# Kernel tuning notes

Measured on AMD Instinct MI355X. Metric: run time of the kernel, lower is better.

Reference implementation:

```python
import jax, jax.numpy as jnp
import numpy as np
import math

N_HEADS = 8
EMBED = 128
HEAD_DEPTH = EMBED // N_HEADS
CLIP = 10.0
NEG_INF = 1.0e10
SCALE = math.sqrt(HEAD_DEPTH)


def setup_inputs() -> dict:
    key = jax.random.key(0)
    ks = jax.random.split(key, 8)
    B, C, N = 32, 2, 512
    Q = jax.random.normal(ks[0], (B, C, N, EMBED), dtype=jnp.float32)
    K = jax.random.normal(ks[1], (B, C, N, EMBED), dtype=jnp.float32)
    V = jax.random.normal(ks[2], (B, C, N, EMBED), dtype=jnp.float32)
    mask = jax.random.bernoulli(ks[3], 0.15, (B, C, N, 1))  # True = masked out
    stdv_qkv = 1.0 / math.sqrt(HEAD_DEPTH)
    stdv_out = 1.0 / math.sqrt(EMBED)
    # torch nn.Linear weights: (out_features, in_features)
    Wq = jax.random.uniform(ks[4], (EMBED, EMBED), jnp.float32, -stdv_qkv, stdv_qkv)
    Wk = jax.random.uniform(ks[5], (EMBED, EMBED), jnp.float32, -stdv_qkv, stdv_qkv)
    Wv = jax.random.uniform(ks[6], (EMBED, EMBED), jnp.float32, -stdv_qkv, stdv_qkv)
    Wout = jax.random.uniform(ks[7], (EMBED, EMBED), jnp.float32, -stdv_out, stdv_out)
    return {"Q": Q, "K": K, "V": V, "mask": mask,
            "Wq": Wq, "Wk": Wk, "Wv": Wv, "Wout": Wout}


def _split_heads(T):
    # (b, c, n, E) -> (b, H, c, n, d)
    b, c, n, _ = T.shape
    return T.reshape(b, c, n, N_HEADS, HEAD_DEPTH).transpose(0, 3, 1, 2, 4)


def reference(Q, K, V, mask, Wq, Wk, Wv, Wout):
    # Linear projections (torch Linear: y = x @ W.T)
    q = _split_heads(jnp.einsum('bcne,fe->bcnf', Q, Wq))
    k = _split_heads(jnp.einsum('bcne,fe->bcnf', K, Wk))
    v = _split_heads(jnp.einsum('bcne,fe->bcnf', V, Wv))
    # logits: (b, H, c, q, k)
    logits = jnp.einsum('bhcqd,bhckd->bhcqk', q, k) / SCALE
    logits = CLIP * jnp.tanh(logits)
    # mask (b, c, n, 1) -> (b, 1, c, 1, n); True -> -1e10
    m = mask[:, None, :, :, :].swapaxes(-1, -2)
    logits = jnp.where(m, -NEG_INF, logits)
    probs = jax.nn.softmax(logits, axis=-1)
    out = jnp.einsum('bhcqk,bhckd->bhcqd', probs, v)
    # combine heads: (b, H, c, n, d) -> (b, c, n, E)
    b, h, c, n, d = out.shape
    out = out.transpose(0, 2, 3, 1, 4).reshape(b, c, n, EMBED)
    return jnp.einsum('bcne,fe->bcnf', out, Wout)
```

## Files before the change

kernel.cpp:

```cpp
#include <hip/hip_runtime.h>

typedef _Float16 half_t;
typedef _Float16 half8 __attribute__((ext_vector_type(8)));
typedef _Float16 half4 __attribute__((ext_vector_type(4)));
typedef float floatx4 __attribute__((ext_vector_type(4)));
typedef float floatx16 __attribute__((ext_vector_type(16)));

#define C1 0.72134752044448170368f
#define C2 14.4269504088896340736f
#define C3 28.8539008177792681472f

__device__ __forceinline__ floatx4 zero4() {
    floatx4 z; z[0] = z[1] = z[2] = z[3] = 0.f; return z;
}
__device__ __forceinline__ floatx16 zero16() {
    floatx16 z;
#pragma unroll
    for (int i = 0; i < 16; ++i) z[i] = 0.f;
    return z;
}

__device__ __forceinline__ float pfun(float sp, float b) {
    float u = __builtin_amdgcn_exp2f(sp);
    float r = __builtin_amdgcn_rcpf(u + 1.0f);
    return __builtin_amdgcn_exp2f(b - C3 * r);
}

__global__ void k_convw(const float* __restrict__ Wq, const float* __restrict__ Wk,
                        const float* __restrict__ Wv, const float* __restrict__ Wo,
                        half_t* __restrict__ Wh) {
    int idx = blockIdx.x * 256 + threadIdx.x;
    int which = idx >> 14;
    int off = idx & 16383;
    const float* src = (which == 0) ? Wq : (which == 1) ? Wk : (which == 2) ? Wv : Wo;
    float scale = (which == 0) ? C1 : 1.0f;
    Wh[idx] = (half_t)(src[off] * scale);
}

__global__ __launch_bounds__(256) void k_proj(
        const float* __restrict__ Q, const float* __restrict__ K,
        const float* __restrict__ V, const half_t* __restrict__ WhBase,
        half_t* __restrict__ qw, half_t* __restrict__ kw, half_t* __restrict__ vw) {
    int which = blockIdx.y;
    const float* X = (which == 0) ? Q : (which == 1) ? K : V;
    const half_t* W = WhBase + which * 16384;

    int tid = threadIdx.x;
    int w = tid >> 6, lane = tid & 63;
    int l15 = lane & 15, quad = lane >> 4;
    int tokbase = blockIdx.x * 64 + w * 16;

    floatx4 acc[8];
#pragma unroll
    for (int nt = 0; nt < 8; ++nt) acc[nt] = zero4();

#pragma unroll
    for (int ks = 0; ks < 4; ++ks) {
        const float* ap = X + (tokbase + l15) * 128 + ks * 32 + quad * 8;
        float4 a0 = *(const float4*)ap;
        float4 a1 = *(const float4*)(ap + 4);
        half8 xf;
        xf[0] = (half_t)a0.x; xf[1] = (half_t)a0.y; xf[2] = (half_t)a0.z; xf[3] = (half_t)a0.w;
        xf[4] = (half_t)a1.x; xf[5] = (half_t)a1.y; xf[6] = (half_t)a1.z; xf[7] = (half_t)a1.w;
        if (which == 2) {
#pragma unroll
            for (int nt = 0; nt < 8; ++nt) {
                half8 wf = *(const half8*)(W + (nt * 16 + l15) * 128 + ks * 32 + quad * 8);
                acc[nt] = __builtin_amdgcn_mfma_f32_16x16x32_f16(xf, wf, acc[nt], 0, 0, 0);
            }
        } else {
#pragma unroll
            for (int nt = 0; nt < 8; ++nt) {
                half8 wf = *(const half8*)(W + (nt * 16 + l15) * 128 + ks * 32 + quad * 8);
                acc[nt] = __builtin_amdgcn_mfma_f32_16x16x32_f16(wf, xf, acc[nt], 0, 0, 0);
            }
        }
    }

    if (which == 2) {
        int R0 = tokbase + quad * 4;
        int bc = R0 >> 9, n0 = R0 & 511;
#pragma unroll
        for (int nt = 0; nt < 8; ++nt) {
            half4 hv;
            hv[0] = (half_t)acc[nt][0]; hv[1] = (half_t)acc[nt][1];
            hv[2] = (half_t)acc[nt][2]; hv[3] = (half_t)acc[nt][3];
            *(half4*)(vw + ((bc * 8 + nt) * 16 + l15) * 512 + n0) = hv;
        }
    } else {
        int R = tokbase + l15;
        int bc = R >> 9, n = R & 511;
        half_t* Y = (which == 0) ? qw : kw;
#pragma unroll
        for (int nt = 0; nt < 8; ++nt) {
            half4 hv;
            hv[0] = (half_t)acc[nt][0]; hv[1] = (half_t)acc[nt][1];
            hv[2] = (half_t)acc[nt][2]; hv[3] = (half_t)acc[nt][3];
            *(half4*)(Y + ((bc * 8 + nt) * 512 + n) * 16 + quad * 4) = hv;
        }
    }
}

__global__ __launch_bounds__(64, 8) void k_attn(
        const half_t* __restrict__ qg, const half_t* __restrict__ kg,
        const half_t* __restrict__ vTg, const int* __restrict__ mask,
        half_t* __restrict__ attn) {
    __shared__ float bias[512];
    __shared__ half_t Pb[32 * 36];

    int bx = blockIdx.x;
    int bch = bx >> 4, qt = bx & 15;
    int bc = bch >> 3, h = bch & 7;
    int lane = threadIdx.x;
    int l31 = lane & 31, hf = lane >> 5;
    int l15 = lane & 15, quad = lane >> 4;

    const half_t* qh = qg + bch * 8192;
    const half_t* kh = kg + bch * 8192;
    const half_t* vh = vTg + bch * 8192;

#pragma unroll
    for (int i = 0; i < 8; ++i)
        bias[i * 64 + lane] = mask[bc * 512 + i * 64 + lane] ? -1.0e30f : C2;
    __syncthreads();

    int qbase = qt * 32;
    half8 qf = *(const half8*)(qh + (qbase + l31) * 16 + hf * 8);

    half8 ones;
#pragma unroll
    for (int j = 0; j < 8; ++j) ones[j] = (half_t)1.0f;

    floatx4 O[2], Os[2];
    O[0] = zero4(); O[1] = zero4();
    Os[0] = zero4(); Os[1] = zero4();
    const float4* b4 = (const float4*)bias;

#pragma unroll 1
    for (int c = 0; c < 16; ++c) {
        half8 kf = *(const half8*)(kh + (c * 32 + l31) * 16 + hf * 8);
        half8 vf = *(const half8*)(vh + l15 * 512 + c * 32 + quad * 8);
        float4 bv[4];
#pragma unroll
        for (int g = 0; g < 4; ++g) bv[g] = b4[c * 8 + hf + 2 * g];

        floatx16 S = __builtin_amdgcn_mfma_f32_32x32x16_f16(kf, qf, zero16(), 0, 0, 0);
#pragma unroll
        for (int g = 0; g < 4; ++g) {
            float p0 = pfun(S[4 * g + 0], bv[g].x);
            float p1 = pfun(S[4 * g + 1], bv[g].y);
            float p2 = pfun(S[4 * g + 2], bv[g].z);
            float p3 = pfun(S[4 * g + 3], bv[g].w);
            auto t0 = __builtin_amdgcn_cvt_pkrtz(p0, p1);
            auto t1 = __builtin_amdgcn_cvt_pkrtz(p2, p3);
            half4 ph;
            ph[0] = (half_t)t0[0]; ph[1] = (half_t)t0[1];
            ph[2] = (half_t)t1[0]; ph[3] = (half_t)t1[1];
            *(half4*)(Pb + l31 * 36 + hf * 4 + g * 8) = ph;
        }
#pragma unroll
        for (int nt2 = 0; nt2 < 2; ++nt2) {
            half8 pb = *(const half8*)(Pb + (nt2 * 16 + l15) * 36 + quad * 8);
            O[nt2]  = __builtin_amdgcn_mfma_f32_16x16x32_f16(vf,   pb, O[nt2],  0, 0, 0);
            Os[nt2] = __builtin_amdgcn_mfma_f32_16x16x32_f16(ones, pb, Os[nt2], 0, 0, 0);
        }
    }

#pragma unroll
    for (int nt = 0; nt < 2; ++nt) {
        float iv = __builtin_amdgcn_rcpf(Os[nt][0]);
        int qrow = qbase + nt * 16 + l15;
        half4 ov;
        ov[0] = (half_t)(O[nt][0] * iv);
        ov[1] = (half_t)(O[nt][1] * iv);
        ov[2] = (half_t)(O[nt][2] * iv);
        ov[3] = (half_t)(O[nt][3] * iv);
        *(half4*)(attn + (bc * 512 + qrow) * 128 + h * 16 + quad * 4) = ov;
    }
}

__global__ __launch_bounds__(256) void k_out(
        const half_t* __restrict__ A, const half_t* __restrict__ Wh,
        float* __restrict__ out) {
    int tid = threadIdx.x;
    int w = tid >> 6, lane = tid & 63;
    int l15 = lane & 15, quad = lane >> 4;
    int tokbase = blockIdx.x * 64 + w * 16;

    floatx4 acc[8];
#pragma unroll
    for (int nt = 0; nt < 8; ++nt) acc[nt] = zero4();
#pragma unroll
    for (int ks = 0; ks < 4; ++ks) {
        half8 xf = *(const half8*)(A + (tokbase + l15) * 128 + ks * 32 + quad * 8);
#pragma unroll
        for (int nt = 0; nt < 8; ++nt) {
            half8 wf = *(const half8*)(Wh + (nt * 16 + l15) * 128 + ks * 32 + quad * 8);
            acc[nt] = __builtin_amdgcn_mfma_f32_16x16x32_f16(wf, xf, acc[nt], 0, 0, 0);
        }
    }
#pragma unroll
    for (int nt = 0; nt < 8; ++nt) {
        float4 o;
        o.x = acc[nt][0]; o.y = acc[nt][1]; o.z = acc[nt][2]; o.w = acc[nt][3];
        *(float4*)(out + (tokbase + l15) * 128 + nt * 16 + quad * 4) = o;
    }
}

extern "C" void kernel_launch(void* const* d_in, const int* in_sizes, int n_in,
                              void* d_out, int out_size, void* d_ws, size_t ws_size,
                              hipStream_t stream) {
    const float* Q    = (const float*)d_in[0];
    const float* K    = (const float*)d_in[1];
    const float* V    = (const float*)d_in[2];
    const int*   mask = (const int*)d_in[3];
    const float* Wq   = (const float*)d_in[4];
    const float* Wk   = (const float*)d_in[5];
    const float* Wv   = (const float*)d_in[6];
    const float* Wo   = (const float*)d_in[7];
    float* out = (float*)d_out;

    half_t* ws = (half_t*)d_ws;
    half_t* Wh = ws;
    half_t* qw = ws + 65536;
    half_t* kw = qw + 4194304;
    half_t* vw = kw + 4194304;
    half_t* aw = vw + 4194304;

    k_convw<<<256, 256, 0, stream>>>(Wq, Wk, Wv, Wo, Wh);
    k_proj<<<dim3(512, 3), 256, 0, stream>>>(Q, K, V, Wh, qw, kw, vw);
    k_attn<<<8192, 64, 0, stream>>>(qw, kw, vw, mask, aw);
    k_out<<<512, 256, 0, stream>>>(aw, Wh + 49152, out);
}
```

Baseline: 180.1 us.

## Drop weight-convert kernel, prefetch K/V in attention, use two-wave attention blocks

Result: slower. 209.4 us (+16.3%).

```diff
diff --git a/kernel.cpp b/kernel.cpp
--- a/kernel.cpp
+++ b/kernel.cpp
@@ -26,24 +26,24 @@
     return __builtin_amdgcn_exp2f(b - C3 * r);
 }
 
-__global__ void k_convw(const float* __restrict__ Wq, const float* __restrict__ Wk,
-                        const float* __restrict__ Wv, const float* __restrict__ Wo,
-                        half_t* __restrict__ Wh) {
-    int idx = blockIdx.x * 256 + threadIdx.x;
-    int which = idx >> 14;
-    int off = idx & 16383;
-    const float* src = (which == 0) ? Wq : (which == 1) ? Wk : (which == 2) ? Wv : Wo;
-    float scale = (which == 0) ? C1 : 1.0f;
-    Wh[idx] = (half_t)(src[off] * scale);
+__device__ __forceinline__ half8 cvt_frag(const float* p) {
+    float4 a0 = *(const float4*)p;
+    float4 a1 = *(const float4*)(p + 4);
+    half8 f;
+    f[0] = (half_t)a0.x; f[1] = (half_t)a0.y; f[2] = (half_t)a0.z; f[3] = (half_t)a0.w;
+    f[4] = (half_t)a1.x; f[5] = (half_t)a1.y; f[6] = (half_t)a1.z; f[7] = (half_t)a1.w;
+    return f;
 }
 
 __global__ __launch_bounds__(256) void k_proj(
         const float* __restrict__ Q, const float* __restrict__ K,
-        const float* __restrict__ V, const half_t* __restrict__ WhBase,
+        const float* __restrict__ V, const float* __restrict__ Wq,
+        const float* __restrict__ Wk, const float* __restrict__ Wv,
         half_t* __restrict__ qw, half_t* __restrict__ kw, half_t* __restrict__ vw) {
     int which = blockIdx.y;
-    const float* X = (which == 0) ? Q : (which == 1) ? K : V;
-    const half_t* W = WhBase + which * 16384;
+    const float* X  = (which == 0) ? Q  : (which == 1) ? K  : V;
+    const float* Wf = (which == 0) ? Wq : (which == 1) ? Wk : Wv;
+    float xs = (which == 0) ? C1 : 1.0f;
 
     int tid = threadIdx.x;
     int w = tid >> 6, lane = tid & 63;
@@ -60,18 +60,20 @@
         float4 a0 = *(const float4*)ap;
         float4 a1 = *(const float4*)(ap + 4);
         half8 xf;
-        xf[0] = (half_t)a0.x; xf[1] = (half_t)a0.y; xf[2] = (half_t)a0.z; xf[3] = (half_t)a0.w;
-        xf[4] = (half_t)a1.x; xf[5] = (half_t)a1.y; xf[6] = (half_t)a1.z; xf[7] = (half_t)a1.w;
+        xf[0] = (half_t)(a0.x * xs); xf[1] = (half_t)(a0.y * xs);
+        xf[2] = (half_t)(a0.z * xs); xf[3] = (half_t)(a0.w * xs);
+        xf[4] = (half_t)(a1.x * xs); xf[5] = (half_t)(a1.y * xs);
+        xf[6] = (half_t)(a1.z * xs); xf[7] = (half_t)(a1.w * xs);
         if (which == 2) {
 #pragma unroll
             for (int nt = 0; nt < 8; ++nt) {
-                half8 wf = *(const half8*)(W + (nt * 16 + l15) * 128 + ks * 32 + quad * 8);
+                half8 wf = cvt_frag(Wf + (nt * 16 + l15) * 128 + ks * 32 + quad * 8);
                 acc[nt] = __builtin_amdgcn_mfma_f32_16x16x32_f16(xf, wf, acc[nt], 0, 0, 0);
             }
         } else {
 #pragma unroll
             for (int nt = 0; nt < 8; ++nt) {
-                half8 wf = *(const half8*)(W + (nt * 16 + l15) * 128 + ks * 32 + quad * 8);
+                half8 wf = cvt_frag(Wf + (nt * 16 + l15) * 128 + ks * 32 + quad * 8);
                 acc[nt] = __builtin_amdgcn_mfma_f32_16x16x32_f16(wf, xf, acc[nt], 0, 0, 0);
             }
         }
@@ -101,17 +103,18 @@
     }
 }
 
-__global__ __launch_bounds__(64, 8) void k_attn(
+__global__ __launch_bounds__(128, 8) void k_attn(
         const half_t* __restrict__ qg, const half_t* __restrict__ kg,
         const half_t* __restrict__ vTg, const int* __restrict__ mask,
         half_t* __restrict__ attn) {
     __shared__ float bias[512];
-    __shared__ half_t Pb[32 * 36];
+    __shared__ half_t Pl[2][32 * 36];
 
     int bx = blockIdx.x;
-    int bch = bx >> 4, qt = bx & 15;
+    int bch = bx >> 3, qe = bx & 7;
     int bc = bch >> 3, h = bch & 7;
-    int lane = threadIdx.x;
+    int tid = threadIdx.x;
+    int w = tid >> 6, lane = tid & 63;
     int l31 = lane & 31, hf = lane >> 5;
     int l15 = lane & 15, quad = lane >> 4;
 
@@ -120,11 +123,11 @@
     const half_t* vh = vTg + bch * 8192;
 
 #pragma unroll
-    for (int i = 0; i < 8; ++i)
-        bias[i * 64 + lane] = mask[bc * 512 + i * 64 + lane] ? -1.0e30f : C2;
+    for (int i = 0; i < 4; ++i)
+        bias[i * 128 + tid] = mask[bc * 512 + i * 128 + tid] ? -1.0e30f : C2;
     __syncthreads();
 
-    int qbase = qt * 32;
+    int qbase = qe * 64 + w * 32;
     half8 qf = *(const half8*)(qh + (qbase + l31) * 16 + hf * 8);
 
     half8 ones;
@@ -134,12 +137,19 @@
     floatx4 O[2], Os[2];
     O[0] = zero4(); O[1] = zero4();
     Os[0] = zero4(); Os[1] = zero4();
+    half_t* Pw = &Pl[w][0];
     const float4* b4 = (const float4*)bias;
+
+    half8 kf = *(const half8*)(kh + l31 * 16 + hf * 8);
+    half8 vf = *(const half8*)(vh + l15 * 512 + quad * 8);
 
 #pragma unroll 1
     for (int c = 0; c < 16; ++c) {
-        half8 kf = *(const half8*)(kh + (c * 32 + l31) * 16 + hf * 8);
-        half8 vf = *(const half8*)(vh + l15 * 512 + c * 32 + quad * 8);
+        half8 kf_n, vf_n;
+        if (c < 15) {
+            kf_n = *(const half8*)(kh + ((c + 1) * 32 + l31) * 16 + hf * 8);
+            vf_n = *(const half8*)(vh + l15 * 512 + (c + 1) * 32 + quad * 8);
+        }
         float4 bv[4];
 #pragma unroll
         for (int g = 0; g < 4; ++g) bv[g] = b4[c * 8 + hf + 2 * g];
@@ -156,14 +166,15 @@
             half4 ph;
             ph[0] = (half_t)t0[0]; ph[1] = (half_t)t0[1];
             ph[2] = (half_t)t1[0]; ph[3] = (half_t)t1[1];
-            *(half4*)(Pb + l31 * 36 + hf * 4 + g * 8) = ph;
+            *(half4*)(Pw + l31 * 36 + hf * 4 + g * 8) = ph;
         }
 #pragma unroll
         for (int nt2 = 0; nt2 < 2; ++nt2) {
-            half8 pb = *(const half8*)(Pb + (nt2 * 16 + l15) * 36 + quad * 8);
+            half8 pb = *(const half8*)(Pw + (nt2 * 16 + l15) * 36 + quad * 8);
             O[nt2]  = __builtin_amdgcn_mfma_f32_16x16x32_f16(vf,   pb, O[nt2],  0, 0, 0);
             Os[nt2] = __builtin_amdgcn_mfma_f32_16x16x32_f16(ones, pb, Os[nt2], 0, 0, 0);
         }
+        kf = kf_n; vf = vf_n;
     }
 
 #pragma unroll
@@ -180,7 +191,7 @@
 }
 
 __global__ __launch_bounds__(256) void k_out(
-        const half_t* __restrict__ A, const half_t* __restrict__ Wh,
+        const half_t* __restrict__ A, const float* __restrict__ Wo,
         float* __restrict__ out) {
     int tid = threadIdx.x;
     int w = tid >> 6, lane = tid & 63;
@@ -195,7 +206,7 @@
         half8 xf = *(const half8*)(A + (tokbase + l15) * 128 + ks * 32 + quad * 8);
 #pragma unroll
         for (int nt = 0; nt < 8; ++nt) {
-            half8 wf = *(const half8*)(Wh + (nt * 16 + l15) * 128 + ks * 32 + quad * 8);
+            half8 wf = cvt_frag(Wo + (nt * 16 + l15) * 128 + ks * 32 + quad * 8);
             acc[nt] = __builtin_amdgcn_mfma_f32_16x16x32_f16(wf, xf, acc[nt], 0, 0, 0);
         }
     }
@@ -221,14 +232,12 @@
     float* out = (float*)d_out;
 
     half_t* ws = (half_t*)d_ws;
-    half_t* Wh = ws;
-    half_t* qw = ws + 65536;
+    half_t* qw = ws;
     half_t* kw = qw + 4194304;
     half_t* vw = kw + 4194304;
     half_t* aw = vw + 4194304;
 
-    k_convw<<<256, 256, 0, stream>>>(Wq, Wk, Wv, Wo, Wh);
-    k_proj<<<dim3(512, 3), 256, 0, stream>>>(Q, K, V, Wh, qw, kw, vw);
-    k_attn<<<8192, 64, 0, stream>>>(qw, kw, vw, mask, aw);
-    k_out<<<512, 256, 0, stream>>>(aw, Wh + 49152, out);
-}
+    k_proj<<<dim3(512, 3), 256, 0, stream>>>(Q, K, V, Wq, Wk, Wv, qw, kw, vw);
+    k_attn<<<4096, 128, 0, stream>>>(qw, kw, vw, mask, aw);
+    k_out<<<512, 256, 0, stream>>>(aw, Wo, out);
+}
```
